# Optimization experiments

Hardware: AMD Instinct MI355X
Metric: run time of the kernel (lower is better)

## Reference

```python
import jax, jax.numpy as jnp
import numpy as np

B, IN, OUT, D = 8192, 1024, 1024, 8


def setup_inputs() -> dict:
    key = jax.random.key(0)
    k1, k2, k3, k4 = jax.random.split(key, 4)
    # kaiming-uniform-ish init for weights, uniform for biases (values don't affect correctness)
    bound = 1.0 / np.sqrt(IN)
    return {
        "input": jax.random.normal(k1, (B, IN), dtype=jnp.float32),
        "w": jax.random.uniform(k2, (B, D), dtype=jnp.float32),
        "weights": jax.random.uniform(k3, (D, OUT, IN), dtype=jnp.float32, minval=-bound, maxval=bound),
        "biases": jax.random.uniform(k4, (D, OUT), dtype=jnp.float32, minval=-bound, maxval=bound),
    }


def reference(input, w, weights, biases):
    # Original math: weight[b] = sum_d w[b,d] * weights[d]  (shape [out,in])
    #                out[b]    = input[b] @ weight[b].T + sum_d w[b,d]*biases[d]
    # Restructured as one big GEMM + cheap dsize reduction:
    # tmp[b,d,o] = sum_i input[b,i] * weights[d,o,i]   (GEMM: [B,in] x [in, d*out])
    tmp = jnp.einsum('bi,doi->bdo', input, weights)
    out = jnp.einsum('bdo,bd->bo', tmp, w) + w @ biases
    return out
```

## Files before the change

kernel.cpp:

```cpp
#include <hip/hip_runtime.h>
#include <stdint.h>

typedef unsigned short u16;
typedef float v4f __attribute__((ext_vector_type(4)));
typedef short v8s __attribute__((ext_vector_type(8)));

#define B_   8192
#define IN_  1024
#define OUT_ 1024
#define D_   8

#define BM 128
#define BN 128
#define BK 64

__device__ __forceinline__ uint32_t cvtpk(float lo, float hi) {
  uint32_t r;
  asm("v_cvt_pk_bf16_f32 %0, %1, %2" : "=v"(r) : "v"(lo), "v"(hi));
  return r;
}

__global__ __launch_bounds__(256) void convert_w(
    const float* __restrict__ weights, u16* __restrict__ wtBf) {
  const int i8 = blockIdx.x * 256 + threadIdx.x;
  const float4* src = (const float4*)weights + (size_t)i8 * 2;
  float4 a = src[0], b = src[1];
  uint4 o;
  o.x = cvtpk(a.x, a.y); o.y = cvtpk(a.z, a.w);
  o.z = cvtpk(b.x, b.y); o.w = cvtpk(b.z, b.w);
  ((uint4*)wtBf)[i8] = o;
}

__device__ __forceinline__ void gload_lds16(const u16* g, u16* l) {
  typedef __attribute__((address_space(1))) void gvoid;
  typedef __attribute__((address_space(3))) void lvoid;
  __builtin_amdgcn_global_load_lds((gvoid*)g, (lvoid*)l, 16, 0, 0);
}

__global__ __launch_bounds__(256) void gemm_fused(
    const float* __restrict__ Ain,
    const u16* __restrict__ Wt,
    const float* __restrict__ w,
    const float* __restrict__ biases,
    float* __restrict__ out) {
  __shared__ __align__(16) u16 As[BM * BK];
  __shared__ __align__(16) u16 Bs[BN * BK];

  const int id   = blockIdx.x;
  const int xcd  = id & 7;
  const int slot = id >> 3;
  const int by   = xcd + ((slot & 7) << 3);
  const int bx   = slot >> 3;

  const int tid  = threadIdx.x;
  const int wid  = tid >> 6;
  const int lane = tid & 63;
  const int wr   = wid >> 1, wc = wid & 1;
  const int quad = lane >> 4, l16 = lane & 15;
  const int m0   = by * BM;
  const int n0   = bx * BN;

  const int swz  = (lane & 7) ^ ((lane >> 3) & 7);
  const int rowS = wid * 32 + (lane >> 3);
  const float* aBase[4];
  const u16*   bBase[4];
  uint32_t*    lA[4];
  u16*         lB[4];
#pragma unroll
  for (int j = 0; j < 4; ++j) {
    const int row = rowS + j * 8;
    aBase[j] = Ain + (size_t)(m0 + row) * IN_ + swz * 8;
    bBase[j] = Wt  + (size_t)(n0 + row) * IN_ + swz * 8;
    const int c = wid * 256 + j * 64 + lane;
    lA[j] = (uint32_t*)(As + c * 8);
    lB[j] = Bs + c * 8;
  }

  const int aRow = wr * 64 + l16;
  const int bRow = wc * 64 + l16;
  const int e    = l16 & 7;
  int aC[2];
#pragma unroll
  for (int h = 0; h < 2; ++h) aC[h] = ((quad + 4 * h) ^ e) * 8;

  const v4f vzero = {0.f, 0.f, 0.f, 0.f};
  v4f acc[4][4];
#pragma unroll
  for (int mt = 0; mt < 4; ++mt)
#pragma unroll
    for (int nt = 0; nt < 4; ++nt) acc[mt][nt] = vzero;

  for (int dd = 0; dd < D_; ++dd) {
    const size_t bOffG = (size_t)dd * OUT_ * IN_;
    float ws[4];
#pragma unroll
    for (int j = 0; j < 4; ++j)
      ws[j] = w[(size_t)(m0 + rowS + j * 8) * D_ + dd];

    for (int it = 0; it < IN_ / BK; ++it) {
      const int i0 = it * BK;
      float4 a0[4], a1[4];
#pragma unroll
      for (int j = 0; j < 4; ++j) {
        const float4* ap = (const float4*)(aBase[j] + i0);
        a0[j] = ap[0];
        a1[j] = ap[1];
      }
#pragma unroll
      for (int j = 0; j < 4; ++j) gload_lds16(bBase[j] + bOffG + i0, lB[j]);
#pragma unroll
      for (int j = 0; j < 4; ++j) {
        const float s = ws[j];
        uint4 pk;
        pk.x = cvtpk(a0[j].x * s, a0[j].y * s);
        pk.y = cvtpk(a0[j].z * s, a0[j].w * s);
        pk.z = cvtpk(a1[j].x * s, a1[j].y * s);
        pk.w = cvtpk(a1[j].z * s, a1[j].w * s);
        *(uint4*)lA[j] = pk;
      }
      __builtin_amdgcn_s_waitcnt(0);
      __syncthreads();

#pragma unroll
      for (int h = 0; h < 2; ++h) {
        v8s af[4], bf[4];
#pragma unroll
        for (int mt = 0; mt < 4; ++mt)
          af[mt] = *(const v8s*)(As + (aRow + mt * 16) * BK + aC[h]);
#pragma unroll
        for (int nt = 0; nt < 4; ++nt)
          bf[nt] = *(const v8s*)(Bs + (bRow + nt * 16) * BK + aC[h]);
#pragma unroll
        for (int mt = 0; mt < 4; ++mt)
#pragma unroll
          for (int nt = 0; nt < 4; ++nt)
            acc[mt][nt] = __builtin_amdgcn_mfma_f32_16x16x32_bf16(
                af[mt], bf[nt], acc[mt][nt], 0, 0, 0);
      }
      __syncthreads();
    }
  }

  float bcol[4][8];
#pragma unroll
  for (int nt = 0; nt < 4; ++nt) {
    const int col = n0 + wc * 64 + nt * 16 + l16;
#pragma unroll
    for (int dd = 0; dd < 8; ++dd) bcol[nt][dd] = biases[dd * OUT_ + col];
  }
#pragma unroll
  for (int mt = 0; mt < 4; ++mt) {
#pragma unroll
    for (int r = 0; r < 4; ++r) {
      const int grow = m0 + wr * 64 + mt * 16 + quad * 4 + r;
      const v4f* wp = (const v4f*)(w + (size_t)grow * D_);
      const v4f wa = wp[0], wb = wp[1];
#pragma unroll
      for (int nt = 0; nt < 4; ++nt) {
        const int col = n0 + wc * 64 + nt * 16 + l16;
        const float bias = wa[0] * bcol[nt][0] + wa[1] * bcol[nt][1] +
                           wa[2] * bcol[nt][2] + wa[3] * bcol[nt][3] +
                           wb[0] * bcol[nt][4] + wb[1] * bcol[nt][5] +
                           wb[2] * bcol[nt][6] + wb[3] * bcol[nt][7];
        out[(size_t)grow * OUT_ + col] = acc[mt][nt][r] + bias;
      }
    }
  }
}

extern "C" void kernel_launch(void* const* d_in, const int* in_sizes, int n_in,
                              void* d_out, int out_size, void* d_ws, size_t ws_size,
                              hipStream_t stream) {
  const float* input   = (const float*)d_in[0];
  const float* w       = (const float*)d_in[1];
  const float* weights = (const float*)d_in[2];
  const float* biases  = (const float*)d_in[3];
  float* out = (float*)d_out;

  u16* wtBf = (u16*)d_ws;

  const int nThreads = (D_ * OUT_ * IN_) / 8;
  convert_w<<<dim3(nThreads / 256), 256, 0, stream>>>(weights, wtBf);
  gemm_fused<<<dim3(512), 256, 0, stream>>>(input, wtBf, w, biases, out);
}
```

Before: 273.6 us.

## Double-buffer LDS and reorder loops so input tiles are loaded once per k-step

```diff
diff --git a/kernel.cpp b/kernel.cpp
--- a/kernel.cpp
+++ b/kernel.cpp
@@ -14,6 +14,12 @@
 #define BN 128
 #define BK 64
 
+__device__ __forceinline__ u16 f2bf(float f) {
+  uint32_t u = __float_as_uint(f);
+  u += 0x7fffu + ((u >> 16) & 1u);
+  return (u16)(u >> 16);
+}
+
 __device__ __forceinline__ uint32_t cvtpk(float lo, float hi) {
   uint32_t r;
   asm("v_cvt_pk_bf16_f32 %0, %1, %2" : "=v"(r) : "v"(lo), "v"(hi));
@@ -22,13 +28,11 @@
 
 __global__ __launch_bounds__(256) void convert_w(
     const float* __restrict__ weights, u16* __restrict__ wtBf) {
-  const int i8 = blockIdx.x * 256 + threadIdx.x;
-  const float4* src = (const float4*)weights + (size_t)i8 * 2;
-  float4 a = src[0], b = src[1];
-  uint4 o;
-  o.x = cvtpk(a.x, a.y); o.y = cvtpk(a.z, a.w);
-  o.z = cvtpk(b.x, b.y); o.w = cvtpk(b.z, b.w);
-  ((uint4*)wtBf)[i8] = o;
+  const int i4 = blockIdx.x * 256 + threadIdx.x;
+  float4 v = ((const float4*)weights)[i4];
+  ushort4 o;
+  o.x = f2bf(v.x); o.y = f2bf(v.y); o.z = f2bf(v.z); o.w = f2bf(v.w);
+  ((ushort4*)wtBf)[i4] = o;
 }
 
 __device__ __forceinline__ void gload_lds16(const u16* g, u16* l) {
@@ -37,14 +41,14 @@
   __builtin_amdgcn_global_load_lds((gvoid*)g, (lvoid*)l, 16, 0, 0);
 }
 
-__global__ __launch_bounds__(256) void gemm_fused(
+__global__ __launch_bounds__(256, 2) void gemm_fused(
     const float* __restrict__ Ain,
     const u16* __restrict__ Wt,
     const float* __restrict__ w,
     const float* __restrict__ biases,
     float* __restrict__ out) {
-  __shared__ __align__(16) u16 As[BM * BK];
-  __shared__ __align__(16) u16 Bs[BN * BK];
+  __shared__ __align__(16) u16 As[2][BM * BK];
+  __shared__ __align__(16) u16 Bs[2][BN * BK];
 
   const int id   = blockIdx.x;
   const int xcd  = id & 7;
@@ -64,16 +68,21 @@
   const int rowS = wid * 32 + (lane >> 3);
   const float* aBase[4];
   const u16*   bBase[4];
-  uint32_t*    lA[4];
-  u16*         lB[4];
+  int cOff[4];
 #pragma unroll
   for (int j = 0; j < 4; ++j) {
     const int row = rowS + j * 8;
     aBase[j] = Ain + (size_t)(m0 + row) * IN_ + swz * 8;
     bBase[j] = Wt  + (size_t)(n0 + row) * IN_ + swz * 8;
-    const int c = wid * 256 + j * 64 + lane;
-    lA[j] = (uint32_t*)(As + c * 8);
-    lB[j] = Bs + c * 8;
+    cOff[j]  = (wid * 256 + j * 64 + lane) * 8;
+  }
+
+  float4 wA[4], wB[4];
+#pragma unroll
+  for (int j = 0; j < 4; ++j) {
+    const float* wp = w + (size_t)(m0 + rowS + j * 8) * D_;
+    wA[j] = ((const float4*)wp)[0];
+    wB[j] = ((const float4*)wp)[1];
   }
 
   const int aRow = wr * 64 + l16;
@@ -90,46 +99,60 @@
 #pragma unroll
     for (int nt = 0; nt < 4; ++nt) acc[mt][nt] = vzero;
 
-  for (int dd = 0; dd < D_; ++dd) {
-    const size_t bOffG = (size_t)dd * OUT_ * IN_;
-    float ws[4];
-#pragma unroll
-    for (int j = 0; j < 4; ++j)
-      ws[j] = w[(size_t)(m0 + rowS + j * 8) * D_ + dd];
-
-    for (int it = 0; it < IN_ / BK; ++it) {
-      const int i0 = it * BK;
-      float4 a0[4], a1[4];
-#pragma unroll
-      for (int j = 0; j < 4; ++j) {
-        const float4* ap = (const float4*)(aBase[j] + i0);
-        a0[j] = ap[0];
-        a1[j] = ap[1];
-      }
-#pragma unroll
-      for (int j = 0; j < 4; ++j) gload_lds16(bBase[j] + bOffG + i0, lB[j]);
-#pragma unroll
-      for (int j = 0; j < 4; ++j) {
-        const float s = ws[j];
-        uint4 pk;
-        pk.x = cvtpk(a0[j].x * s, a0[j].y * s);
-        pk.y = cvtpk(a0[j].z * s, a0[j].w * s);
-        pk.z = cvtpk(a1[j].x * s, a1[j].y * s);
-        pk.w = cvtpk(a1[j].z * s, a1[j].w * s);
-        *(uint4*)lA[j] = pk;
-      }
-      __builtin_amdgcn_s_waitcnt(0);
-      __syncthreads();
+  float4 a0[4], a1[4];
+
+#pragma unroll
+  for (int j = 0; j < 4; ++j) {
+    const float4* ap = (const float4*)aBase[j];
+    a0[j] = ap[0]; a1[j] = ap[1];
+  }
+#pragma unroll
+  for (int j = 0; j < 4; ++j) gload_lds16(bBase[j], &Bs[0][cOff[j]]);
+#pragma unroll
+  for (int j = 0; j < 4; ++j) {
+    const float s = wA[j].x;
+    uint4 pk;
+    pk.x = cvtpk(a0[j].x * s, a0[j].y * s);
+    pk.y = cvtpk(a0[j].z * s, a0[j].w * s);
+    pk.z = cvtpk(a1[j].x * s, a1[j].y * s);
+    pk.w = cvtpk(a1[j].z * s, a1[j].w * s);
+    *(uint4*)(&As[0][cOff[j]]) = pk;
+  }
+  __builtin_amdgcn_s_waitcnt(0);
+  __syncthreads();
+
+  for (int it = 0; it < IN_ / BK; ++it) {
+#pragma unroll
+    for (int dd = 0; dd < D_; ++dd) {
+      const int cur = dd & 1;
+      const int nxt = cur ^ 1;
+      const int sdd = (dd + 1) & 7;
+      const bool last = (it == IN_ / BK - 1) && (dd == D_ - 1);
+
+      if (!last) {
+        const int sit = (dd == D_ - 1) ? it + 1 : it;
+        if (dd == D_ - 1) {
+#pragma unroll
+          for (int j = 0; j < 4; ++j) {
+            const float4* ap = (const float4*)(aBase[j] + sit * BK);
+            a0[j] = ap[0]; a1[j] = ap[1];
+          }
+        }
+#pragma unroll
+        for (int j = 0; j < 4; ++j)
+          gload_lds16(bBase[j] + (size_t)sdd * (OUT_ * IN_) + sit * BK,
+                      &Bs[nxt][cOff[j]]);
+      }
 
 #pragma unroll
       for (int h = 0; h < 2; ++h) {
         v8s af[4], bf[4];
 #pragma unroll
         for (int mt = 0; mt < 4; ++mt)
-          af[mt] = *(const v8s*)(As + (aRow + mt * 16) * BK + aC[h]);
+          af[mt] = *(const v8s*)(&As[cur][(aRow + mt * 16) * BK + aC[h]]);
 #pragma unroll
         for (int nt = 0; nt < 4; ++nt)
-          bf[nt] = *(const v8s*)(Bs + (bRow + nt * 16) * BK + aC[h]);
+          bf[nt] = *(const v8s*)(&Bs[cur][(bRow + nt * 16) * BK + aC[h]]);
 #pragma unroll
         for (int mt = 0; mt < 4; ++mt)
 #pragma unroll
@@ -137,6 +160,20 @@
             acc[mt][nt] = __builtin_amdgcn_mfma_f32_16x16x32_bf16(
                 af[mt], bf[nt], acc[mt][nt], 0, 0, 0);
       }
+
+      if (!last) {
+#pragma unroll
+        for (int j = 0; j < 4; ++j) {
+          const float s = (sdd < 4) ? wA[j][sdd] : wB[j][sdd - 4];
+          uint4 pk;
+          pk.x = cvtpk(a0[j].x * s, a0[j].y * s);
+          pk.y = cvtpk(a0[j].z * s, a0[j].w * s);
+          pk.z = cvtpk(a1[j].x * s, a1[j].y * s);
+          pk.w = cvtpk(a1[j].z * s, a1[j].w * s);
+          *(uint4*)(&As[nxt][cOff[j]]) = pk;
+        }
+      }
+      __builtin_amdgcn_s_waitcnt(0);
       __syncthreads();
     }
   }
@@ -179,7 +216,7 @@
 
   u16* wtBf = (u16*)d_ws;
 
-  const int nThreads = (D_ * OUT_ * IN_) / 8;
-  convert_w<<<dim3(nThreads / 256), 256, 0, stream>>>(weights, wtBf);
+  const int nF4 = (D_ * OUT_ * IN_) / 4;
+  convert_w<<<dim3(nF4 / 256), 256, 0, stream>>>(weights, wtBf);
   gemm_fused<<<dim3(512), 256, 0, stream>>>(input, wtBf, w, biases, out);
 }
```

Result: faster. 233.7 us (-14.6%).
